# Performance work log

Measured on AMD Instinct MI355X. Metric: run time of the kernel, lower is better.

## Reference

```python
import jax, jax.numpy as jnp
import numpy as np

N_NODES = 10000
N_EDGES = 320000
D_IN = 256
D_HID = 256
N_CLASSES = 40


def _init_linear(key, fan_in, fan_out):
    kw, kb = jax.random.split(key)
    bound = 1.0 / np.sqrt(fan_in)
    W = jax.random.uniform(kw, (fan_in, fan_out), jnp.float32, -bound, bound)
    b = jax.random.uniform(kb, (fan_out,), jnp.float32, -bound, bound)
    return W, b


def setup_inputs() -> dict:
    key = jax.random.key(0)
    k0, k1, k2, k3, k4 = jax.random.split(key, 5)
    node_features = jax.random.normal(k0, (N_NODES, D_IN), jnp.float32)
    edge_index = jax.random.randint(k1, (2, N_EDGES), 0, N_NODES, jnp.int64)
    W1, b1 = _init_linear(k2, D_IN, D_HID)
    W2, b2 = _init_linear(k3, D_HID, D_HID)
    W3, b3 = _init_linear(k4, D_HID, N_CLASSES)
    return {"node_features": node_features, "edge_index": edge_index,
            "W1": W1, "b1": b1, "W2": W2, "b2": b2, "W3": W3, "b3": b3}


def _mp_layer(x, src, dst, W, b):
    # message: linear transform of source-node features (transform-then-gather
    # is mathematically identical to gather-then-transform and cheaper when E>N)
    msg = (x @ W + b)[src]                      # [E, d_out]
    # scatter sum-aggregate messages at destination nodes
    out = jax.ops.segment_sum(msg, dst, num_segments=N_NODES)  # [N, d_out]
    return out


def reference(node_features, edge_index, W1, b1, W2, b2, W3, b3):
    src, dst = edge_index[0], edge_index[1]
    x = jax.nn.relu(_mp_layer(node_features, src, dst, W1, b1))
    x = jax.nn.relu(_mp_layer(x, src, dst, W2, b2))
    x = jax.nn.relu(_mp_layer(x, src, dst, W3, b3))
    return x
```

## Files before the change

kernel.cpp:

```cpp
#include <hip/hip_runtime.h>


#define N_NODES   10000
#define N_EDGES   320000
#define D_HID     256
#define N_CLASSES 40
#define CAP       96

typedef __attribute__((ext_vector_type(8))) short short8;
typedef __attribute__((ext_vector_type(4))) float f32x4;

__device__ __forceinline__ ushort f2bf(float f) {
    unsigned u = __float_as_uint(f);
    u = (u + 0x7fffu + ((u >> 16) & 1u)) >> 16;
    return (ushort)u;
}
__device__ __forceinline__ float bf2f(ushort u) {
    return __uint_as_float(((unsigned)u) << 16);
}


__global__ __launch_bounds__(256)
void prep_kernel(const float* __restrict__ X,
                 const float* __restrict__ W1, const float* __restrict__ W2,
                 const float* __restrict__ W3,
                 ushort* __restrict__ Xb, ushort* __restrict__ bufY,
                 ushort* __restrict__ bufH,
                 ushort* __restrict__ W1b, ushort* __restrict__ W2b,
                 ushort* __restrict__ W3b, int* __restrict__ cursor,
                 int* __restrict__ esrc) {
    const int tid  = blockIdx.x * 256 + threadIdx.x;
    const int nthr = gridDim.x * 256;
    for (int i = tid; i < N_NODES; i += nthr) cursor[i] = 0;
    for (int i = tid; i < N_NODES * CAP; i += nthr) esrc[i] = N_NODES;
    ushort4 z; z.x = 0; z.y = 0; z.z = 0; z.w = 0;
    if (tid < 64) {
        ((ushort4*)Xb)[640000 + tid]   = z;
        ((ushort4*)bufY)[640000 + tid] = z;
    }
    if (tid < 10) ((ushort4*)bufH)[100000 + tid] = z;
    for (int i = tid; i < N_NODES * D_HID / 4; i += nthr) {
        float4 v = ((const float4*)X)[i];
        ushort4 o;
        o.x = f2bf(v.x); o.y = f2bf(v.y); o.z = f2bf(v.z); o.w = f2bf(v.w);
        ((ushort4*)Xb)[i] = o;
    }
    for (int i = tid; i < 141312; i += nthr) {
        if (i < 65536) {
            int n = i >> 8, k = i & 255;
            W1b[i] = f2bf(W1[k * 256 + n]);
        } else if (i < 131072) {
            int t2 = i - 65536;
            int n = t2 >> 8, k = t2 & 255;
            W2b[t2] = f2bf(W2[k * 256 + n]);
        } else {
            int t2 = i - 131072;
            int n = t2 >> 8, k = t2 & 255;
            W3b[t2] = f2bf(W3[k * N_CLASSES + n]);
        }
    }
}


__global__ __launch_bounds__(256)
void place_kernel(const int* __restrict__ edges, int* __restrict__ cursor,
                  int* __restrict__ esrc) {
    int e = blockIdx.x * 256 + threadIdx.x;
    if (e < N_EDGES) {
        int d = edges[N_EDGES + e];
        int pos = atomicAdd(&cursor[d], 1);
        if (pos < CAP) esrc[d * CAP + pos] = edges[e];
    }
}


#define LDSA 264

template<bool CHAIN>
__global__ __launch_bounds__(256)
void layer_kernel(const ushort* __restrict__ Xin, const ushort* __restrict__ Bt,
                  const float* __restrict__ bias,
                  const int* __restrict__ deg, const int* __restrict__ esrc,
                  const ushort* __restrict__ W3b, const float* __restrict__ b3,
                  ushort* __restrict__ Out) {
    __shared__ ushort As[16 * LDSA];
    __shared__ ushort Bs[40 * LDSA];
    __shared__ int    eidxL[16 * CAP];
    __shared__ int    degI[16];
    __shared__ float  degF[16];

    const int tid = threadIdx.x;
    const int wave = tid >> 6, lane = tid & 63;
    const int lr = lane & 15, lg = lane >> 4;
    const int rowBase = blockIdx.x * 16;

#pragma unroll
    for (int p = 0; p < 6; ++p) {
        int idx = p * 256 + tid;
        eidxL[idx] = esrc[rowBase * CAP + idx];
    }
    if (tid < 16) {
        int c = deg[rowBase + tid];
        degF[tid] = (float)c;
        degI[tid] = (c > CAP) ? CAP : c;
    }
    __syncthreads();

    const uint2* hp = (const uint2*)Xin;
#pragma unroll 1
    for (int it = 0; it < 4; ++it) {
        int nl = wave * 4 + it;
        int cntp = (degI[nl] + 7) & ~7;
        float a0 = 0.f, a1 = 0.f, a2 = 0.f, a3 = 0.f;
#pragma unroll 1
        for (int i = 0; i < cntp; i += 8) {
            uint2 v[8];
#pragma unroll
            for (int u = 0; u < 8; ++u) {
                int s = eidxL[nl * CAP + i + u];
                v[u] = hp[(size_t)s * 64 + lane];
            }
#pragma unroll
            for (int u = 0; u < 8; ++u) {
                a0 += bf2f((ushort)(v[u].x & 0xffff));
                a1 += bf2f((ushort)(v[u].x >> 16));
                a2 += bf2f((ushort)(v[u].y & 0xffff));
                a3 += bf2f((ushort)(v[u].y >> 16));
            }
        }
        uint2 o;
        o.x = (unsigned)f2bf(a0) | ((unsigned)f2bf(a1) << 16);
        o.y = (unsigned)f2bf(a2) | ((unsigned)f2bf(a3) << 16);
        *(uint2*)(As + nl * LDSA + lane * 4) = o;
    }

    f32x4 acc[4] = {};
    for (int k0 = 0; k0 < 256; k0 += 32) {
        __syncthreads();
#pragma unroll
        for (int p = 0; p < 4; ++p) {
            int idx = p * 256 + tid;
            int n = idx >> 2, c = (idx & 3) * 8;
            *(uint4*)(Bs + n * 40 + c) = *(const uint4*)(Bt + (size_t)n * 256 + k0 + c);
        }
        __syncthreads();
        short8 af = *(const short8*)(As + lr * LDSA + k0 + lg * 8);
#pragma unroll
        for (int j = 0; j < 4; ++j) {
            short8 bf = *(const short8*)(Bs + (wave * 64 + j * 16 + lr) * 40 + lg * 8);
            acc[j] = __builtin_amdgcn_mfma_f32_16x16x32_bf16(af, bf, acc[j], 0, 0, 0);
        }
    }

    if (!CHAIN) {
#pragma unroll
        for (int j = 0; j < 4; ++j) {
            int col = wave * 64 + j * 16 + lr;
            float bv = bias[col];
#pragma unroll
            for (int r = 0; r < 4; ++r) {
                int grow = rowBase + lg * 4 + r;
                float dg = degF[lg * 4 + r];
                Out[(size_t)grow * 256 + col] = f2bf(fmaxf(fmaf(dg, bv, acc[j][r]), 0.f));
            }
        }
    } else {
        __syncthreads();
#pragma unroll
        for (int j = 0; j < 4; ++j) {
            int col = wave * 64 + j * 16 + lr;
            float bv = bias[col];
#pragma unroll
            for (int r = 0; r < 4; ++r) {
                int rl = lg * 4 + r;
                As[rl * LDSA + col] = f2bf(fmaxf(fmaf(degF[rl], bv, acc[j][r]), 0.f));
            }
        }
#pragma unroll
        for (int p = 0; p < 5; ++p) {
            int idx = p * 256 + tid;
            int n = idx >> 5, c = (idx & 31) * 8;
            *(uint4*)(Bs + n * LDSA + c) = *(const uint4*)(W3b + (size_t)n * 256 + c);
        }
        __syncthreads();
        if (wave < 3) {
            f32x4 acc3 = {};
            for (int k0 = 0; k0 < 256; k0 += 32) {
                short8 af = *(const short8*)(As + lr * LDSA + k0 + lg * 8);
                short8 bf = *(const short8*)(Bs + (wave * 16 + lr) * LDSA + k0 + lg * 8);
                acc3 = __builtin_amdgcn_mfma_f32_16x16x32_bf16(af, bf, acc3, 0, 0, 0);
            }
            int col = wave * 16 + lr;
            if (col < N_CLASSES) {
                float bv = b3[col];
#pragma unroll
                for (int r = 0; r < 4; ++r) {
                    int grow = rowBase + lg * 4 + r;
                    Out[(size_t)grow * N_CLASSES + col] = f2bf(acc3[r] + bv);
                }
            }
        }
    }
}


__global__ __launch_bounds__(256)
void agg_relu_40_kernel(const ushort* __restrict__ h, const int* __restrict__ deg,
                        const int* __restrict__ esrc, float* __restrict__ out) {
    int wv   = threadIdx.x >> 6;
    int lane = threadIdx.x & 63;
    int node = (blockIdx.x << 2) + wv;
    if (node >= N_NODES) return;
    int cnt = deg[node];
    if (cnt > CAP) cnt = CAP;
    int cntp = (cnt + 7) & ~7;
    const int* ep = esrc + node * CAP;
    if (lane < N_CLASSES) {
        float a = 0.f, b = 0.f;
#pragma unroll 1
        for (int i = 0; i < cntp; i += 8) {
            int s[8];
#pragma unroll
            for (int u = 0; u < 8; ++u) s[u] = ep[i + u];
#pragma unroll
            for (int u = 0; u < 8; u += 2) {
                a += bf2f(h[(size_t)s[u]     * N_CLASSES + lane]);
                b += bf2f(h[(size_t)s[u + 1] * N_CLASSES + lane]);
            }
        }
        out[(size_t)node * N_CLASSES + lane] = fmaxf(a + b, 0.f);
    }
}


extern "C" void kernel_launch(void* const* d_in, const int* in_sizes, int n_in,
                              void* d_out, int out_size, void* d_ws, size_t ws_size,
                              hipStream_t stream) {
    const float* X     = (const float*)d_in[0];
    const int*   edges = (const int*)d_in[1];
    const float* W1 = (const float*)d_in[2];
    const float* b1 = (const float*)d_in[3];
    const float* W2 = (const float*)d_in[4];
    const float* b2 = (const float*)d_in[5];
    const float* W3 = (const float*)d_in[6];
    const float* b3 = (const float*)d_in[7];
    float* out = (float*)d_out;

    char* ws = (char*)d_ws;
    ushort* Xb   = (ushort*)(ws);
    ushort* bufY = (ushort*)(ws + 5120512);
    ushort* bufH = (ushort*)(ws + 10241024);
    ushort* W1b  = (ushort*)(ws + 11041104);
    ushort* W2b  = (ushort*)(ws + 11172176);
    ushort* W3b  = (ushort*)(ws + 11303248);
    int*   cursor = (int*)(ws + 11323728);
    int*   esrc   = (int*)(ws + 11363728);

    prep_kernel<<<512, 256, 0, stream>>>(X, W1, W2, W3, Xb, bufY, bufH,
                                         W1b, W2b, W3b, cursor, esrc);
    place_kernel<<<(N_EDGES + 255) / 256, 256, 0, stream>>>(edges, cursor, esrc);
    layer_kernel<false><<<N_NODES / 16, 256, 0, stream>>>(
        Xb, W1b, b1, cursor, esrc, W3b, b3, bufY);
    layer_kernel<true><<<N_NODES / 16, 256, 0, stream>>>(
        bufY, W2b, b2, cursor, esrc, W3b, b3, bufH);
    agg_relu_40_kernel<<<(N_NODES + 3) / 4, 256, 0, stream>>>(bufH, cursor, esrc, out);
}
```

Baseline: 160.3 us.

## Use 1024-thread blocks with one wave per node and drop esrc padding fill

Layer blocks grow from 4 to 16 waves, so each wave gathers one destination node instead of four and computes one 16-column MFMA tile instead of four. The prep kernel no longer fills the padded edge list with a sentinel; readers instead substitute the zero row index for slots beyond the degree. This removes roughly 3.8 MB of initialisation writes and raises the number of gathers in flight per block. In exchange it adds per-slot bounds checks and larger blocks with more barrier participants, which may reduce how many blocks fit per CU.

Result: slower. 174.2 us (+8.7%).

```diff
diff --git a/kernel.cpp b/kernel.cpp
--- a/kernel.cpp
+++ b/kernel.cpp
@@ -27,12 +27,10 @@
                  ushort* __restrict__ Xb, ushort* __restrict__ bufY,
                  ushort* __restrict__ bufH,
                  ushort* __restrict__ W1b, ushort* __restrict__ W2b,
-                 ushort* __restrict__ W3b, int* __restrict__ cursor,
-                 int* __restrict__ esrc) {
+                 ushort* __restrict__ W3b, int* __restrict__ cursor) {
     const int tid  = blockIdx.x * 256 + threadIdx.x;
     const int nthr = gridDim.x * 256;
     for (int i = tid; i < N_NODES; i += nthr) cursor[i] = 0;
-    for (int i = tid; i < N_NODES * CAP; i += nthr) esrc[i] = N_NODES;
     ushort4 z; z.x = 0; z.y = 0; z.z = 0; z.w = 0;
     if (tid < 64) {
         ((ushort4*)Xb)[640000 + tid]   = z;
@@ -77,7 +75,7 @@
 #define LDSA 264
 
 template<bool CHAIN>
-__global__ __launch_bounds__(256)
+__global__ __launch_bounds__(1024)
 void layer_kernel(const ushort* __restrict__ Xin, const ushort* __restrict__ Bt,
                   const float* __restrict__ bias,
                   const int* __restrict__ deg, const int* __restrict__ esrc,
@@ -94,10 +92,11 @@
     const int lr = lane & 15, lg = lane >> 4;
     const int rowBase = blockIdx.x * 16;
 
-#pragma unroll
-    for (int p = 0; p < 6; ++p) {
-        int idx = p * 256 + tid;
-        eidxL[idx] = esrc[rowBase * CAP + idx];
+    {
+        int idx = tid;
+        if (idx < 16 * CAP) eidxL[idx] = esrc[rowBase * CAP + idx];
+        idx = 1024 + tid;
+        if (idx < 16 * CAP) eidxL[idx] = esrc[rowBase * CAP + idx];
     }
     if (tid < 16) {
         int c = deg[rowBase + tid];
@@ -107,17 +106,17 @@
     __syncthreads();
 
     const uint2* hp = (const uint2*)Xin;
-#pragma unroll 1
-    for (int it = 0; it < 4; ++it) {
-        int nl = wave * 4 + it;
-        int cntp = (degI[nl] + 7) & ~7;
+    {
+        const int cnt  = degI[wave];
+        const int cntp = (cnt + 7) & ~7;
         float a0 = 0.f, a1 = 0.f, a2 = 0.f, a3 = 0.f;
 #pragma unroll 1
         for (int i = 0; i < cntp; i += 8) {
             uint2 v[8];
 #pragma unroll
             for (int u = 0; u < 8; ++u) {
-                int s = eidxL[nl * CAP + i + u];
+                int slot = i + u;
+                int s = (slot < cnt) ? eidxL[wave * CAP + slot] : N_NODES;
                 v[u] = hp[(size_t)s * 64 + lane];
             }
 #pragma unroll
@@ -131,56 +130,53 @@
         uint2 o;
         o.x = (unsigned)f2bf(a0) | ((unsigned)f2bf(a1) << 16);
         o.y = (unsigned)f2bf(a2) | ((unsigned)f2bf(a3) << 16);
-        *(uint2*)(As + nl * LDSA + lane * 4) = o;
-    }
-
-    f32x4 acc[4] = {};
+        *(uint2*)(As + wave * LDSA + lane * 4) = o;
+    }
+
+    f32x4 acc = {};
     for (int k0 = 0; k0 < 256; k0 += 32) {
         __syncthreads();
-#pragma unroll
-        for (int p = 0; p < 4; ++p) {
-            int idx = p * 256 + tid;
-            int n = idx >> 2, c = (idx & 3) * 8;
+        {
+            int n = tid >> 2, c = (tid & 3) * 8;
             *(uint4*)(Bs + n * 40 + c) = *(const uint4*)(Bt + (size_t)n * 256 + k0 + c);
         }
         __syncthreads();
         short8 af = *(const short8*)(As + lr * LDSA + k0 + lg * 8);
-#pragma unroll
-        for (int j = 0; j < 4; ++j) {
-            short8 bf = *(const short8*)(Bs + (wave * 64 + j * 16 + lr) * 40 + lg * 8);
-            acc[j] = __builtin_amdgcn_mfma_f32_16x16x32_bf16(af, bf, acc[j], 0, 0, 0);
-        }
+        short8 bf = *(const short8*)(Bs + (wave * 16 + lr) * 40 + lg * 8);
+        acc = __builtin_amdgcn_mfma_f32_16x16x32_bf16(af, bf, acc, 0, 0, 0);
     }
 
     if (!CHAIN) {
-#pragma unroll
-        for (int j = 0; j < 4; ++j) {
-            int col = wave * 64 + j * 16 + lr;
-            float bv = bias[col];
-#pragma unroll
-            for (int r = 0; r < 4; ++r) {
-                int grow = rowBase + lg * 4 + r;
-                float dg = degF[lg * 4 + r];
-                Out[(size_t)grow * 256 + col] = f2bf(fmaxf(fmaf(dg, bv, acc[j][r]), 0.f));
-            }
+        int col = wave * 16 + lr;
+        float bv = bias[col];
+#pragma unroll
+        for (int r = 0; r < 4; ++r) {
+            int grow = rowBase + lg * 4 + r;
+            float dg = degF[lg * 4 + r];
+            Out[(size_t)grow * 256 + col] = f2bf(fmaxf(fmaf(dg, bv, acc[r]), 0.f));
         }
     } else {
         __syncthreads();
-#pragma unroll
-        for (int j = 0; j < 4; ++j) {
-            int col = wave * 64 + j * 16 + lr;
+        {
+            int col = wave * 16 + lr;
             float bv = bias[col];
 #pragma unroll
             for (int r = 0; r < 4; ++r) {
                 int rl = lg * 4 + r;
-                As[rl * LDSA + col] = f2bf(fmaxf(fmaf(degF[rl], bv, acc[j][r]), 0.f));
-            }
-        }
-#pragma unroll
-        for (int p = 0; p < 5; ++p) {
-            int idx = p * 256 + tid;
-            int n = idx >> 5, c = (idx & 31) * 8;
-            *(uint4*)(Bs + n * LDSA + c) = *(const uint4*)(W3b + (size_t)n * 256 + c);
+                As[rl * LDSA + col] = f2bf(fmaxf(fmaf(degF[rl], bv, acc[r]), 0.f));
+            }
+        }
+        {
+            int idx = tid;
+            if (idx < 1280) {
+                int n = idx >> 5, c = (idx & 31) * 8;
+                *(uint4*)(Bs + n * LDSA + c) = *(const uint4*)(W3b + (size_t)n * 256 + c);
+            }
+            idx = 1024 + tid;
+            if (idx < 1280) {
+                int n = idx >> 5, c = (idx & 31) * 8;
+                *(uint4*)(Bs + n * LDSA + c) = *(const uint4*)(W3b + (size_t)n * 256 + c);
+            }
         }
         __syncthreads();
         if (wave < 3) {
@@ -221,7 +217,7 @@
         for (int i = 0; i < cntp; i += 8) {
             int s[8];
 #pragma unroll
-            for (int u = 0; u < 8; ++u) s[u] = ep[i + u];
+            for (int u = 0; u < 8; ++u) s[u] = (i + u < cnt) ? ep[i + u] : N_NODES;
 #pragma unroll
             for (int u = 0; u < 8; u += 2) {
                 a += bf2f(h[(size_t)s[u]     * N_CLASSES + lane]);
@@ -257,11 +253,11 @@
     int*   esrc   = (int*)(ws + 11363728);
 
     prep_kernel<<<512, 256, 0, stream>>>(X, W1, W2, W3, Xb, bufY, bufH,
-                                         W1b, W2b, W3b, cursor, esrc);
+                                         W1b, W2b, W3b, cursor);
     place_kernel<<<(N_EDGES + 255) / 256, 256, 0, stream>>>(edges, cursor, esrc);
-    layer_kernel<false><<<N_NODES / 16, 256, 0, stream>>>(
+    layer_kernel<false><<<N_NODES / 16, 1024, 0, stream>>>(
         Xb, W1b, b1, cursor, esrc, W3b, b3, bufY);
-    layer_kernel<true><<<N_NODES / 16, 256, 0, stream>>>(
+    layer_kernel<true><<<N_NODES / 16, 1024, 0, stream>>>(
         bufY, W2b, b2, cursor, esrc, W3b, b3, bufH);
     agg_relu_40_kernel<<<(N_NODES + 3) / 4, 256, 0, stream>>>(bufH, cursor, esrc, out);
 }
```

## Drop esrc sentinel fill and LDS weight staging; read B fragments from global

Applied to the files above, without the earlier changes.

Removes the prep-time fill of the padded edge-slot table (about 3.8 MB of writes) and instead masks slots past the degree to a zero sentinel row inside the gather loops. The layer kernel no longer stages weight tiles in LDS with two barriers per k-step; MFMA B fragments are loaded straight from global/L2, and LDS shrinks so launch bounds can request 8 blocks per CU. The cost is uncoalesced, repeated weight reads from cache for every block instead of shared staging.

Measured after the change: 178.5 us. 1.11x slower.

```diff
diff --git a/kernel.cpp b/kernel.cpp
--- a/kernel.cpp
+++ b/kernel.cpp
@@ -27,12 +27,10 @@
                  ushort* __restrict__ Xb, ushort* __restrict__ bufY,
                  ushort* __restrict__ bufH,
                  ushort* __restrict__ W1b, ushort* __restrict__ W2b,
-                 ushort* __restrict__ W3b, int* __restrict__ cursor,
-                 int* __restrict__ esrc) {
+                 ushort* __restrict__ W3b, int* __restrict__ cursor) {
     const int tid  = blockIdx.x * 256 + threadIdx.x;
     const int nthr = gridDim.x * 256;
     for (int i = tid; i < N_NODES; i += nthr) cursor[i] = 0;
-    for (int i = tid; i < N_NODES * CAP; i += nthr) esrc[i] = N_NODES;
     ushort4 z; z.x = 0; z.y = 0; z.z = 0; z.w = 0;
     if (tid < 64) {
         ((ushort4*)Xb)[640000 + tid]   = z;
@@ -77,14 +75,13 @@
 #define LDSA 264
 
 template<bool CHAIN>
-__global__ __launch_bounds__(256)
+__global__ __launch_bounds__(256, 8)
 void layer_kernel(const ushort* __restrict__ Xin, const ushort* __restrict__ Bt,
                   const float* __restrict__ bias,
                   const int* __restrict__ deg, const int* __restrict__ esrc,
                   const ushort* __restrict__ W3b, const float* __restrict__ b3,
                   ushort* __restrict__ Out) {
     __shared__ ushort As[16 * LDSA];
-    __shared__ ushort Bs[40 * LDSA];
     __shared__ int    eidxL[16 * CAP];
     __shared__ int    degI[16];
     __shared__ float  degF[16];
@@ -110,14 +107,16 @@
 #pragma unroll 1
     for (int it = 0; it < 4; ++it) {
         int nl = wave * 4 + it;
-        int cntp = (degI[nl] + 7) & ~7;
+        const int cnt  = degI[nl];
+        const int cntp = (cnt + 7) & ~7;
         float a0 = 0.f, a1 = 0.f, a2 = 0.f, a3 = 0.f;
 #pragma unroll 1
         for (int i = 0; i < cntp; i += 8) {
             uint2 v[8];
 #pragma unroll
             for (int u = 0; u < 8; ++u) {
-                int s = eidxL[nl * CAP + i + u];
+                int slot = i + u;
+                int s = (slot < cnt) ? eidxL[nl * CAP + slot] : N_NODES;
                 v[u] = hp[(size_t)s * 64 + lane];
             }
 #pragma unroll
@@ -133,21 +132,16 @@
         o.y = (unsigned)f2bf(a2) | ((unsigned)f2bf(a3) << 16);
         *(uint2*)(As + nl * LDSA + lane * 4) = o;
     }
+    __syncthreads();
 
     f32x4 acc[4] = {};
+#pragma unroll 1
     for (int k0 = 0; k0 < 256; k0 += 32) {
-        __syncthreads();
-#pragma unroll
-        for (int p = 0; p < 4; ++p) {
-            int idx = p * 256 + tid;
-            int n = idx >> 2, c = (idx & 3) * 8;
-            *(uint4*)(Bs + n * 40 + c) = *(const uint4*)(Bt + (size_t)n * 256 + k0 + c);
-        }
-        __syncthreads();
         short8 af = *(const short8*)(As + lr * LDSA + k0 + lg * 8);
 #pragma unroll
         for (int j = 0; j < 4; ++j) {
-            short8 bf = *(const short8*)(Bs + (wave * 64 + j * 16 + lr) * 40 + lg * 8);
+            int col = wave * 64 + j * 16 + lr;
+            short8 bf = *(const short8*)(Bt + (size_t)col * 256 + k0 + lg * 8);
             acc[j] = __builtin_amdgcn_mfma_f32_16x16x32_bf16(af, bf, acc[j], 0, 0, 0);
         }
     }
@@ -176,21 +170,17 @@
                 As[rl * LDSA + col] = f2bf(fmaxf(fmaf(degF[rl], bv, acc[j][r]), 0.f));
             }
         }
-#pragma unroll
-        for (int p = 0; p < 5; ++p) {
-            int idx = p * 256 + tid;
-            int n = idx >> 5, c = (idx & 31) * 8;
-            *(uint4*)(Bs + n * LDSA + c) = *(const uint4*)(W3b + (size_t)n * 256 + c);
-        }
         __syncthreads();
         if (wave < 3) {
+            int col = wave * 16 + lr;
+            int colc = (col < N_CLASSES) ? col : 0;
             f32x4 acc3 = {};
+#pragma unroll 1
             for (int k0 = 0; k0 < 256; k0 += 32) {
                 short8 af = *(const short8*)(As + lr * LDSA + k0 + lg * 8);
-                short8 bf = *(const short8*)(Bs + (wave * 16 + lr) * LDSA + k0 + lg * 8);
+                short8 bf = *(const short8*)(W3b + (size_t)colc * 256 + k0 + lg * 8);
                 acc3 = __builtin_amdgcn_mfma_f32_16x16x32_bf16(af, bf, acc3, 0, 0, 0);
             }
-            int col = wave * 16 + lr;
             if (col < N_CLASSES) {
                 float bv = b3[col];
 #pragma unroll
@@ -221,7 +211,7 @@
         for (int i = 0; i < cntp; i += 8) {
             int s[8];
 #pragma unroll
-            for (int u = 0; u < 8; ++u) s[u] = ep[i + u];
+            for (int u = 0; u < 8; ++u) s[u] = (i + u < cnt) ? ep[i + u] : N_NODES;
 #pragma unroll
             for (int u = 0; u < 8; u += 2) {
                 a += bf2f(h[(size_t)s[u]     * N_CLASSES + lane]);
@@ -257,7 +247,7 @@
     int*   esrc   = (int*)(ws + 11363728);
 
     prep_kernel<<<512, 256, 0, stream>>>(X, W1, W2, W3, Xb, bufY, bufH,
-                                         W1b, W2b, W3b, cursor, esrc);
+                                         W1b, W2b, W3b, cursor);
     place_kernel<<<(N_EDGES + 255) / 256, 256, 0, stream>>>(edges, cursor, esrc);
     layer_kernel<false><<<N_NODES / 16, 256, 0, stream>>>(
         Xb, W1b, b1, cursor, esrc, W3b, b3, bufY);
```
